# Kernel tuning notes

Measured on AMD Instinct MI355X. Metric: run time of the kernel, lower is better.

Reference implementation:

```python
import jax, jax.numpy as jnp
import numpy as np

CHAMFER_WEIGHT = 1.0
REG_WEIGHT = 0.1


def setup_inputs() -> dict:
    key = jax.random.key(0)
    k1, k2, k3 = jax.random.split(key, 3)
    B, N, M, K = 16, 4096, 4096, 64
    return {
        "predicted_points": jax.random.normal(k1, (B, N, 3), dtype=jnp.float32),
        "ground_truth_points": jax.random.normal(k2, (B, M, 3), dtype=jnp.float32),
        "trans_feat": jax.random.normal(k3, (B, K, K), dtype=jnp.float32),
    }


def _chamfer(pred, target):
    # Euclidean (non-squared) pairwise distances, matching torch.cdist.
    # Gram trick avoids materializing [B,N,M,3].
    p2 = jnp.sum(pred * pred, axis=-1)          # [B,N]
    t2 = jnp.sum(target * target, axis=-1)      # [B,M]
    cross = jnp.einsum("bnd,bmd->bnm", pred, target)  # [B,N,M]
    d2 = p2[:, :, None] + t2[:, None, :] - 2.0 * cross
    dist = jnp.sqrt(jnp.maximum(d2, 0.0))       # [B,N,M]
    min1 = jnp.min(dist, axis=2)                # [B,N] pred -> nearest target
    min2 = jnp.min(dist, axis=1)                # [B,M] target -> nearest pred
    return jnp.mean(jnp.mean(min1, axis=1) + jnp.mean(min2, axis=1))


def _feature_transform_reg(trans):
    K = trans.shape[1]
    I = jnp.eye(K, dtype=trans.dtype)
    gram = jnp.einsum("bik,bjk->bij", trans, trans)  # trans @ trans^T
    # Frobenius norm per batch element, then mean over batch
    return jnp.mean(jnp.sqrt(jnp.sum((gram - I) ** 2, axis=(1, 2))))


def reference(predicted_points, ground_truth_points, trans_feat):
    chamfer = _chamfer(predicted_points, ground_truth_points)
    reg = _feature_transform_reg(trans_feat)
    return CHAMFER_WEIGHT * chamfer + REG_WEIGHT * reg
```

## Files before the change

kernel.cpp:

```cpp
#include <hip/hip_runtime.h>
#include <math.h>

#define BB 16
#define NN 4096
#define MM 4096
#define NSLICE 2
#define SLICE_COLS 2048
#define NJT (SLICE_COLS / 64)
#define ROWS_PER_BLOCK 256
#define NCHAMFER 512
#define EPW 2176
#define CSTRIDE 2080
#define WSCOL_OFF (BB * NSLICE * NN)

typedef __attribute__((ext_vector_type(8))) short bf16x8;
typedef __attribute__((ext_vector_type(16))) float f32x16;

static __device__ inline unsigned short f2bf(float f) {
    unsigned int u = __float_as_uint(f);
    return (unsigned short)((u + 0x7FFFu + ((u >> 16) & 1u)) >> 16);
}
static __device__ inline bf16x8 bzero() {
    bf16x8 z;
    #pragma unroll
    for (int i = 0; i < 8; ++i) z[i] = 0;
    return z;
}
static __device__ inline f32x16 fzero16() {
    f32x16 z;
    #pragma unroll
    for (int i = 0; i < 16; ++i) z[i] = 0.f;
    return z;
}
static __device__ inline float min3f(float a, float b, float c) {
    return fminf(fminf(a, b), c);
}
static __device__ inline float colmin32(const f32x16 x, const f32x16 y) {
    float e[32];
    #pragma unroll
    for (int i = 0; i < 16; ++i) { e[i] = x[i]; e[16 + i] = y[i]; }
    float p[11];
    #pragma unroll
    for (int i = 0; i < 10; ++i) p[i] = min3f(e[3*i], e[3*i+1], e[3*i+2]);
    p[10] = fminf(e[30], e[31]);
    const float q0 = min3f(p[0], p[1], p[2]);
    const float q1 = min3f(p[3], p[4], p[5]);
    const float q2 = min3f(p[6], p[7], p[8]);
    const float q3 = fminf(p[9], p[10]);
    return fminf(min3f(q0, q1, q2), q3);
}

#define MFMA32(Af, Bf, Cf) __builtin_amdgcn_mfma_f32_32x32x16_bf16(Af, Bf, Cf, 0, 0, 0)

__global__ __launch_bounds__(256, 2) void chamfer_min_kernel(
    const float* __restrict__ pred, const float* __restrict__ gt,
    float* __restrict__ ws, float* __restrict__ out)
{
    const int bx  = blockIdx.x;
    const int tid = threadIdx.x;
    if (bx == 0 && tid == 0) *out = 0.0f;

    __shared__ __align__(16) float smem[8704];
    __shared__ __align__(16) unsigned short colw[8 * CSTRIDE];

    const int lane = tid & 63;
    const int w    = tid >> 6;
    const int li   = lane & 31;
    const int hi   = lane >> 5;
    const int tile   = bx & 15;
    const int mslice = (bx >> 4) & 1;
    const int b      = bx >> 5;
    const float* rb = pred + (size_t)b * NN * 3;
    const float* cb = gt + ((size_t)b * MM + (size_t)mslice * SLICE_COLS) * 3;

    const int rbase = tile * ROWS_PER_BLOCK + w * 64;
    bf16x8 A0 = bzero(), A1 = bzero();
    if (lane < 32) {
        #pragma unroll
        for (int f = 0; f < 2; ++f) {
            const float* rp = rb + (size_t)(rbase + f * 32 + li) * 3;
            const float px = rp[0], py = rp[1], pz = rp[2];
            const float p2 = px * px + py * py + pz * pz;
            bf16x8 fr = bzero();
            fr[0] = (short)f2bf(-2.f * px);
            fr[1] = (short)f2bf(-2.f * py);
            fr[2] = (short)f2bf(-2.f * pz);
            fr[3] = (short)f2bf(p2);
            fr[4] = (short)0x3F80;
            if (f == 0) A0 = fr; else A1 = fr;
        }
    }

    uint4* sB = (uint4*)smem;
    #pragma unroll
    for (int i = 0; i < SLICE_COLS / 512; ++i) {
        const int c0 = i * 512 + 2 * tid;
        const float2* sp = (const float2*)(cb + (size_t)c0 * 3);
        const float2 v0 = sp[0], v1 = sp[1], v2 = sp[2];
        const float t2a = v0.x * v0.x + v0.y * v0.y + v1.x * v1.x;
        const float t2b = v1.y * v1.y + v2.x * v2.x + v2.y * v2.y;
        uint4 pa, pb;
        pa.x = (unsigned)f2bf(v0.x) | ((unsigned)f2bf(v0.y) << 16);
        pa.y = (unsigned)f2bf(v1.x) | (0x3F80u << 16);
        pa.z = (unsigned)f2bf(t2a);
        pa.w = 0u;
        pb.x = (unsigned)f2bf(v1.y) | ((unsigned)f2bf(v2.x) << 16);
        pb.y = (unsigned)f2bf(v2.y) | (0x3F80u << 16);
        pb.z = (unsigned)f2bf(t2b);
        pb.w = 0u;
        sB[c0]     = pa;
        sB[c0 + 1] = pb;
    }
    __syncthreads();

    float mv0[16], mv1[16];
    #pragma unroll
    for (int r = 0; r < 16; ++r) { mv0[r] = 3.4e38f; mv1[r] = 3.4e38f; }

    const f32x16 Z = fzero16();
    const bf16x8* sBf = (const bf16x8*)smem;
    unsigned short* myplane = &colw[(w * 2 + hi) * CSTRIDE];

    bf16x8 c1 = sBf[li], c2 = sBf[32 + li];
    for (int jt = 0; jt < NJT; ++jt) {
        bf16x8 n1 = c1, n2 = c2;
        if (jt + 1 < NJT) {
            n1 = sBf[(jt + 1) * 64 + li];
            n2 = sBf[(jt + 1) * 64 + 32 + li];
        }
        f32x16 a0 = MFMA32(A0, c1, Z);
        f32x16 a1 = MFMA32(A0, c2, Z);
        f32x16 a2 = MFMA32(A1, c1, Z);
        f32x16 a3 = MFMA32(A1, c2, Z);
        #pragma unroll
        for (int r = 0; r < 16; ++r)
            mv0[r] = min3f(a0[r], a1[r], mv0[r]);
        #pragma unroll
        for (int r = 0; r < 16; ++r)
            mv1[r] = min3f(a2[r], a3[r], mv1[r]);
        myplane[jt * 64 + li]      = f2bf(colmin32(a0, a2));
        myplane[jt * 64 + 32 + li] = f2bf(colmin32(a1, a3));
        c1 = n1; c2 = n2;
    }
    __syncthreads();

    {
        float cm[8];
        #pragma unroll
        for (int j = 0; j < 8; ++j) cm[j] = 3.4e38f;
        #pragma unroll
        for (int p = 0; p < 8; ++p) {
            const uint4 v = *(const uint4*)&colw[p * CSTRIDE + tid * 8];
            cm[0] = fminf(cm[0], __uint_as_float(v.x << 16));
            cm[1] = fminf(cm[1], __uint_as_float(v.x & 0xFFFF0000u));
            cm[2] = fminf(cm[2], __uint_as_float(v.y << 16));
            cm[3] = fminf(cm[3], __uint_as_float(v.y & 0xFFFF0000u));
            cm[4] = fminf(cm[4], __uint_as_float(v.z << 16));
            cm[5] = fminf(cm[5], __uint_as_float(v.z & 0xFFFF0000u));
            cm[6] = fminf(cm[6], __uint_as_float(v.w << 16));
            cm[7] = fminf(cm[7], __uint_as_float(v.w & 0xFFFF0000u));
        }
        float* wc = ws + WSCOL_OFF
                  + (((size_t)b * 16 + tile) * NSLICE + mslice) * SLICE_COLS;
        *(float4*)&wc[tid * 8]     = make_float4(cm[0], cm[1], cm[2], cm[3]);
        *(float4*)&wc[tid * 8 + 4] = make_float4(cm[4], cm[5], cm[6], cm[7]);
    }

    {
        float* wb = smem + w * EPW + li * 68;
        #pragma unroll
        for (int q = 0; q < 4; ++q) {
            const int rl = q * 8 + hi * 4;
            *(float4*)&wb[rl]      = make_float4(mv0[4*q], mv0[4*q+1], mv0[4*q+2], mv0[4*q+3]);
            *(float4*)&wb[rl + 32] = make_float4(mv1[4*q], mv1[4*q+1], mv1[4*q+2], mv1[4*q+3]);
        }
    }
    __syncthreads();
    {
        const int wsrc = tid >> 6, rl = tid & 63;
        const float* rb2 = smem + wsrc * EPW + rl;
        float m = 3.4e38f;
        #pragma unroll
        for (int c = 0; c < 32; c += 2) m = min3f(rb2[c * 68], rb2[(c + 1) * 68], m);
        ws[((size_t)b * NSLICE + mslice) * NN + tile * ROWS_PER_BLOCK + tid] = m;
    }
}

__global__ __launch_bounds__(256) void finish_reg_kernel(
    const float* __restrict__ ws, const float* __restrict__ trans,
    float* __restrict__ out)
{
    const int bx  = blockIdx.x;
    const int tid = threadIdx.x;
    __shared__ float ssum[4];

    if (bx < BB) {
        const int b = bx;
        const float* p0 = ws + ((size_t)b * NSLICE) * NN;
        float s = 0.f;
        #pragma unroll 4
        for (int i = 0; i < NN / 256; ++i) {
            const int n = i * 256 + tid;
            const float v = fminf(p0[n], p0[NN + n]);
            s += sqrtf(fmaxf(v, 0.0f));
        }
        #pragma unroll
        for (int off = 32; off > 0; off >>= 1)
            s += __shfl_down(s, off, 64);
        if ((tid & 63) == 0) ssum[tid >> 6] = s;
        __syncthreads();
        if (tid == 0)
            atomicAdd(out, (ssum[0] + ssum[1] + ssum[2] + ssum[3])
                               * (1.0f / ((float)BB * (float)NN)));
        return;
    }
    if (bx < 2 * BB) {
        const int b = bx - BB;
        const float* base = ws + WSCOL_OFF + (size_t)b * 16 * NSLICE * SLICE_COLS;
        float acc[8];
        #pragma unroll
        for (int j = 0; j < 8; ++j) acc[j] = 3.4e38f;
        #pragma unroll 4
        for (int p = 0; p < 16 * NSLICE; ++p) {
            const float* pl = base + (size_t)p * SLICE_COLS + tid * 8;
            const float4 x = *(const float4*)pl;
            const float4 y = *(const float4*)(pl + 4);
            acc[0] = fminf(acc[0], x.x); acc[1] = fminf(acc[1], x.y);
            acc[2] = fminf(acc[2], x.z); acc[3] = fminf(acc[3], x.w);
            acc[4] = fminf(acc[4], y.x); acc[5] = fminf(acc[5], y.y);
            acc[6] = fminf(acc[6], y.z); acc[7] = fminf(acc[7], y.w);
        }
        float s = 0.f;
        #pragma unroll
        for (int j = 0; j < 8; ++j) s += sqrtf(fmaxf(acc[j], 0.0f));
        #pragma unroll
        for (int off = 32; off > 0; off >>= 1)
            s += __shfl_down(s, off, 64);
        if ((tid & 63) == 0) ssum[tid >> 6] = s;
        __syncthreads();
        if (tid == 0)
            atomicAdd(out, (ssum[0] + ssum[1] + ssum[2] + ssum[3])
                               * (1.0f / ((float)BB * (float)NN)));
        return;
    }

    if (tid < 64) {
        const int b = bx - 2 * BB;
        const int lane = tid;
        const int hi = lane >> 5, li = lane & 31;
        const float* T = trans + (size_t)b * 64 * 64;
        bf16x8 frag[2][4];
        #pragma unroll
        for (int h = 0; h < 2; ++h)
            #pragma unroll
            for (int s = 0; s < 4; ++s) {
                const float* rp = T + (size_t)(h * 32 + li) * 64 + s * 16 + hi * 8;
                const float4 u0 = *(const float4*)rp;
                const float4 u1 = *(const float4*)(rp + 4);
                bf16x8 fr;
                fr[0] = (short)f2bf(u0.x); fr[1] = (short)f2bf(u0.y);
                fr[2] = (short)f2bf(u0.z); fr[3] = (short)f2bf(u0.w);
                fr[4] = (short)f2bf(u1.x); fr[5] = (short)f2bf(u1.y);
                fr[6] = (short)f2bf(u1.z); fr[7] = (short)f2bf(u1.w);
                frag[h][s] = fr;
            }
        float fsum = 0.f;
        #pragma unroll
        for (int fi = 0; fi < 2; ++fi)
            #pragma unroll
            for (int fj = 0; fj < 2; ++fj) {
                f32x16 a = fzero16();
                #pragma unroll
                for (int s = 0; s < 4; ++s)
                    a = MFMA32(frag[fi][s], frag[fj][s], a);
                #pragma unroll
                for (int r = 0; r < 16; ++r) {
                    const int row = fi * 32 + (r & 3) + 8 * (r >> 2) + 4 * hi;
                    const int col = fj * 32 + li;
                    const float d = a[r] - ((row == col) ? 1.0f : 0.0f);
                    fsum = fmaf(d, d, fsum);
                }
            }
        #pragma unroll
        for (int off = 32; off > 0; off >>= 1)
            fsum += __shfl_down(fsum, off, 64);
        if (lane == 0)
            atomicAdd(out, (0.1f / (float)BB) * sqrtf(fsum));
    }
}

extern "C" void kernel_launch(void* const* d_in, const int* in_sizes, int n_in,
                              void* d_out, int out_size, void* d_ws, size_t ws_size,
                              hipStream_t stream)
{
    const float* pred  = (const float*)d_in[0];
    const float* gt    = (const float*)d_in[1];
    const float* trans = (const float*)d_in[2];
    float* out = (float*)d_out;
    float* ws = (float*)d_ws;

    chamfer_min_kernel<<<dim3(NCHAMFER), dim3(256), 0, stream>>>(pred, gt, ws, out);
    finish_reg_kernel<<<dim3(3 * BB), dim3(256), 0, stream>>>(ws, trans, out);
}
```

Before: 27.93 us.

## Split chamfer rows across eight waves and pack column minima as bf16

The chamfer block now runs 512 threads, with each wave owning 32 rows instead of 64. Each wave does two MFMAs per column tile instead of four, which raises wave-level parallelism. Per-tile column minima are reduced with a cross-half lane shuffle and packed two-per-word as bf16 with v_cvt_pk_bf16_f32. The cross-wave and cross-tile column reductions then use integer min on the packed halves, which halves workspace traffic in both kernels. Unsigned integer min on bf16 bit patterns is only order-correct for non-negative values, so slightly negative squared distances are ranked differently. LDS grows to a 64KB shared buffer per block, which limits how many blocks fit per CU.

Result: faster. 27.08 us (-3.0%).

```diff
diff --git a/kernel.cpp b/kernel.cpp
--- a/kernel.cpp
+++ b/kernel.cpp
@@ -9,8 +9,6 @@
 #define NJT (SLICE_COLS / 64)
 #define ROWS_PER_BLOCK 256
 #define NCHAMFER 512
-#define EPW 2176
-#define CSTRIDE 2080
 #define WSCOL_OFF (BB * NSLICE * NN)
 
 typedef __attribute__((ext_vector_type(8))) short bf16x8;
@@ -35,24 +33,20 @@
 static __device__ inline float min3f(float a, float b, float c) {
     return fminf(fminf(a, b), c);
 }
-static __device__ inline float colmin32(const f32x16 x, const f32x16 y) {
-    float e[32];
-    #pragma unroll
-    for (int i = 0; i < 16; ++i) { e[i] = x[i]; e[16 + i] = y[i]; }
-    float p[11];
-    #pragma unroll
-    for (int i = 0; i < 10; ++i) p[i] = min3f(e[3*i], e[3*i+1], e[3*i+2]);
-    p[10] = fminf(e[30], e[31]);
-    const float q0 = min3f(p[0], p[1], p[2]);
-    const float q1 = min3f(p[3], p[4], p[5]);
-    const float q2 = min3f(p[6], p[7], p[8]);
-    const float q3 = fminf(p[9], p[10]);
-    return fminf(min3f(q0, q1, q2), q3);
+static __device__ inline float tree16(const f32x16 x) {
+    const float p0 = min3f(x[0], x[1], x[2]);
+    const float p1 = min3f(x[3], x[4], x[5]);
+    const float p2 = min3f(x[6], x[7], x[8]);
+    const float p3 = min3f(x[9], x[10], x[11]);
+    const float p4 = min3f(x[12], x[13], x[14]);
+    const float q0 = min3f(p0, p1, x[15]);
+    const float q1 = min3f(p2, p3, p4);
+    return fminf(q0, q1);
 }
 
 #define MFMA32(Af, Bf, Cf) __builtin_amdgcn_mfma_f32_32x32x16_bf16(Af, Bf, Cf, 0, 0, 0)
 
-__global__ __launch_bounds__(256, 2) void chamfer_min_kernel(
+__global__ __launch_bounds__(512, 4) void chamfer_min_kernel(
     const float* __restrict__ pred, const float* __restrict__ gt,
     float* __restrict__ ws, float* __restrict__ out)
 {
@@ -60,8 +54,11 @@
     const int tid = threadIdx.x;
     if (bx == 0 && tid == 0) *out = 0.0f;
 
-    __shared__ __align__(16) float smem[8704];
-    __shared__ __align__(16) unsigned short colw[8 * CSTRIDE];
+    __shared__ __align__(16) unsigned char lds[65536];
+    uint4* sB = (uint4*)lds;
+    const bf16x8* sBf = (const bf16x8*)lds;
+    unsigned* colw = (unsigned*)(lds + 32768);
+    float* epi = (float*)lds;
 
     const int lane = tid & 63;
     const int w    = tid >> 6;
@@ -73,28 +70,24 @@
     const float* rb = pred + (size_t)b * NN * 3;
     const float* cb = gt + ((size_t)b * MM + (size_t)mslice * SLICE_COLS) * 3;
 
-    const int rbase = tile * ROWS_PER_BLOCK + w * 64;
-    bf16x8 A0 = bzero(), A1 = bzero();
+    const int rbase = tile * ROWS_PER_BLOCK + w * 32;
+    bf16x8 A0 = bzero();
     if (lane < 32) {
-        #pragma unroll
-        for (int f = 0; f < 2; ++f) {
-            const float* rp = rb + (size_t)(rbase + f * 32 + li) * 3;
-            const float px = rp[0], py = rp[1], pz = rp[2];
-            const float p2 = px * px + py * py + pz * pz;
-            bf16x8 fr = bzero();
-            fr[0] = (short)f2bf(-2.f * px);
-            fr[1] = (short)f2bf(-2.f * py);
-            fr[2] = (short)f2bf(-2.f * pz);
-            fr[3] = (short)f2bf(p2);
-            fr[4] = (short)0x3F80;
-            if (f == 0) A0 = fr; else A1 = fr;
-        }
-    }
-
-    uint4* sB = (uint4*)smem;
-    #pragma unroll
-    for (int i = 0; i < SLICE_COLS / 512; ++i) {
-        const int c0 = i * 512 + 2 * tid;
+        const float* rp = rb + (size_t)(rbase + li) * 3;
+        const float px = rp[0], py = rp[1], pz = rp[2];
+        const float p2 = px * px + py * py + pz * pz;
+        bf16x8 fr = bzero();
+        fr[0] = (short)f2bf(-2.f * px);
+        fr[1] = (short)f2bf(-2.f * py);
+        fr[2] = (short)f2bf(-2.f * pz);
+        fr[3] = (short)f2bf(p2);
+        fr[4] = (short)0x3F80;
+        A0 = fr;
+    }
+
+    #pragma unroll
+    for (int i = 0; i < 2; ++i) {
+        const int c0 = (i * 512 + tid) * 2;
         const float2* sp = (const float2*)(cb + (size_t)c0 * 3);
         const float2 v0 = sp[0], v1 = sp[1], v2 = sp[2];
         const float t2a = v0.x * v0.x + v0.y * v0.y + v1.x * v1.x;
@@ -113,15 +106,15 @@
     }
     __syncthreads();
 
-    float mv0[16], mv1[16];
-    #pragma unroll
-    for (int r = 0; r < 16; ++r) { mv0[r] = 3.4e38f; mv1[r] = 3.4e38f; }
+    float mv[16];
+    #pragma unroll
+    for (int r = 0; r < 16; ++r) mv[r] = 3.4e38f;
 
     const f32x16 Z = fzero16();
-    const bf16x8* sBf = (const bf16x8*)smem;
-    unsigned short* myplane = &colw[(w * 2 + hi) * CSTRIDE];
+    unsigned* myplane = colw + w * 1024;
 
     bf16x8 c1 = sBf[li], c2 = sBf[32 + li];
+    #pragma unroll 2
     for (int jt = 0; jt < NJT; ++jt) {
         bf16x8 n1 = c1, n2 = c2;
         if (jt + 1 < NJT) {
@@ -130,58 +123,53 @@
         }
         f32x16 a0 = MFMA32(A0, c1, Z);
         f32x16 a1 = MFMA32(A0, c2, Z);
-        f32x16 a2 = MFMA32(A1, c1, Z);
-        f32x16 a3 = MFMA32(A1, c2, Z);
         #pragma unroll
         for (int r = 0; r < 16; ++r)
-            mv0[r] = min3f(a0[r], a1[r], mv0[r]);
-        #pragma unroll
-        for (int r = 0; r < 16; ++r)
-            mv1[r] = min3f(a2[r], a3[r], mv1[r]);
-        myplane[jt * 64 + li]      = f2bf(colmin32(a0, a2));
-        myplane[jt * 64 + 32 + li] = f2bf(colmin32(a1, a3));
+            mv[r] = min3f(a0[r], a1[r], mv[r]);
+        float tA = tree16(a0);
+        float tB = tree16(a1);
+        tA = fminf(tA, __shfl_xor(tA, 32, 64));
+        tB = fminf(tB, __shfl_xor(tB, 32, 64));
+        unsigned pk;
+        asm("v_cvt_pk_bf16_f32 %0, %1, %2" : "=v"(pk) : "v"(tA), "v"(tB));
+        if (lane < 32) myplane[jt * 32 + li] = pk;
         c1 = n1; c2 = n2;
     }
     __syncthreads();
 
     {
-        float cm[8];
-        #pragma unroll
-        for (int j = 0; j < 8; ++j) cm[j] = 3.4e38f;
-        #pragma unroll
-        for (int p = 0; p < 8; ++p) {
-            const uint4 v = *(const uint4*)&colw[p * CSTRIDE + tid * 8];
-            cm[0] = fminf(cm[0], __uint_as_float(v.x << 16));
-            cm[1] = fminf(cm[1], __uint_as_float(v.x & 0xFFFF0000u));
-            cm[2] = fminf(cm[2], __uint_as_float(v.y << 16));
-            cm[3] = fminf(cm[3], __uint_as_float(v.y & 0xFFFF0000u));
-            cm[4] = fminf(cm[4], __uint_as_float(v.z << 16));
-            cm[5] = fminf(cm[5], __uint_as_float(v.z & 0xFFFF0000u));
-            cm[6] = fminf(cm[6], __uint_as_float(v.w << 16));
-            cm[7] = fminf(cm[7], __uint_as_float(v.w & 0xFFFF0000u));
-        }
-        float* wc = ws + WSCOL_OFF
-                  + (((size_t)b * 16 + tile) * NSLICE + mslice) * SLICE_COLS;
-        *(float4*)&wc[tid * 8]     = make_float4(cm[0], cm[1], cm[2], cm[3]);
-        *(float4*)&wc[tid * 8 + 4] = make_float4(cm[4], cm[5], cm[6], cm[7]);
-    }
+        unsigned* wc = (unsigned*)(ws + WSCOL_OFF)
+                     + (((size_t)b * 16 + tile) * NSLICE + mslice) * 1024;
+        #pragma unroll
+        for (int i = 0; i < 2; ++i) {
+            const int slot = i * 512 + tid;
+            unsigned la = 0xFFFFu, ha = 0xFFFFu;
+            #pragma unroll
+            for (int p = 0; p < 8; ++p) {
+                const unsigned u = colw[p * 1024 + slot];
+                la = min(la, u & 0xFFFFu);
+                ha = min(ha, u >> 16);
+            }
+            wc[slot] = la | (ha << 16);
+        }
+    }
+    __syncthreads();
 
     {
-        float* wb = smem + w * EPW + li * 68;
-        #pragma unroll
-        for (int q = 0; q < 4; ++q) {
-            const int rl = q * 8 + hi * 4;
-            *(float4*)&wb[rl]      = make_float4(mv0[4*q], mv0[4*q+1], mv0[4*q+2], mv0[4*q+3]);
-            *(float4*)&wb[rl + 32] = make_float4(mv1[4*q], mv1[4*q+1], mv1[4*q+2], mv1[4*q+3]);
-        }
-    }
-    __syncthreads();
-    {
-        const int wsrc = tid >> 6, rl = tid & 63;
-        const float* rb2 = smem + wsrc * EPW + rl;
+        float* wb = epi + w * 1152 + li * 36;
+        #pragma unroll
+        for (int q = 0; q < 4; ++q)
+            *(float4*)&wb[q * 8 + hi * 4] =
+                make_float4(mv[4*q], mv[4*q+1], mv[4*q+2], mv[4*q+3]);
+    }
+    __syncthreads();
+
+    if (tid < ROWS_PER_BLOCK) {
+        const int wsrc = tid >> 5, rl = tid & 31;
+        const float* rr = epi + wsrc * 1152 + rl;
         float m = 3.4e38f;
         #pragma unroll
-        for (int c = 0; c < 32; c += 2) m = min3f(rb2[c * 68], rb2[(c + 1) * 68], m);
+        for (int c = 0; c < 32; c += 2) m = min3f(rr[c * 36], rr[(c + 1) * 36], m);
         ws[((size_t)b * NSLICE + mslice) * NN + tile * ROWS_PER_BLOCK + tid] = m;
     }
 }
@@ -216,23 +204,24 @@
     }
     if (bx < 2 * BB) {
         const int b = bx - BB;
-        const float* base = ws + WSCOL_OFF + (size_t)b * 16 * NSLICE * SLICE_COLS;
-        float acc[8];
-        #pragma unroll
-        for (int j = 0; j < 8; ++j) acc[j] = 3.4e38f;
-        #pragma unroll 4
-        for (int p = 0; p < 16 * NSLICE; ++p) {
-            const float* pl = base + (size_t)p * SLICE_COLS + tid * 8;
-            const float4 x = *(const float4*)pl;
-            const float4 y = *(const float4*)(pl + 4);
-            acc[0] = fminf(acc[0], x.x); acc[1] = fminf(acc[1], x.y);
-            acc[2] = fminf(acc[2], x.z); acc[3] = fminf(acc[3], x.w);
-            acc[4] = fminf(acc[4], y.x); acc[5] = fminf(acc[5], y.y);
-            acc[6] = fminf(acc[6], y.z); acc[7] = fminf(acc[7], y.w);
-        }
+        const unsigned* base = (const unsigned*)(ws + WSCOL_OFF)
+                             + (size_t)b * 16 * NSLICE * 1024;
         float s = 0.f;
         #pragma unroll
-        for (int j = 0; j < 8; ++j) s += sqrtf(fmaxf(acc[j], 0.0f));
+        for (int i = 0; i < 8; ++i) {
+            const int idx = i * 256 + tid;
+            const int sl  = idx >> 10;
+            const int slot = idx & 1023;
+            unsigned la = 0xFFFFu, ha = 0xFFFFu;
+            #pragma unroll
+            for (int t = 0; t < 16; ++t) {
+                const unsigned u = base[((size_t)t * NSLICE + sl) * 1024 + slot];
+                la = min(la, u & 0xFFFFu);
+                ha = min(ha, u >> 16);
+            }
+            s += sqrtf(fmaxf(__uint_as_float(la << 16), 0.0f));
+            s += sqrtf(fmaxf(__uint_as_float(ha << 16), 0.0f));
+        }
         #pragma unroll
         for (int off = 32; off > 0; off >>= 1)
             s += __shfl_down(s, off, 64);
@@ -299,6 +288,6 @@
     float* out = (float*)d_out;
     float* ws = (float*)d_ws;
 
-    chamfer_min_kernel<<<dim3(NCHAMFER), dim3(256), 0, stream>>>(pred, gt, ws, out);
+    chamfer_min_kernel<<<dim3(NCHAMFER), dim3(512), 0, stream>>>(pred, gt, ws, out);
     finish_reg_kernel<<<dim3(3 * BB), dim3(256), 0, stream>>>(ws, trans, out);
 }
```
